# Optimization experiments

Hardware: AMD Instinct MI355X
Metric: run time of the kernel (lower is better)

The kernel has to match this reference:

```python
import math
import jax, jax.numpy as jnp
import numpy as np

B, V, D, H, DE, DFF = 2, 2048, 1024, 16, 256, 4096
DK = D // H


def setup_inputs() -> dict:
    key = jax.random.key(0)
    ks = jax.random.split(key, 24)
    n = lambda k, shape, s=0.02: (jax.random.normal(k, shape, jnp.float32) * s)
    z = lambda *shape: jnp.zeros(shape, jnp.float32)
    return {
        'x': jax.random.normal(ks[0], (B, V, D), jnp.float32),
        'e_node': jax.random.normal(ks[1], (B, V, DE), jnp.float32),
        'conn': jax.random.uniform(ks[2], (B, V, V), jnp.float32),
        'ln1_g': jnp.ones((D,), jnp.float32), 'ln1_b': z(D),
        'f1w1': n(ks[3], (DE, 2 * D)), 'f1b1': z(2 * D),
        'f1w2': n(ks[4], (2 * D, 2 * D)), 'f1b2': z(2 * D),
        'wq': n(ks[5], (D, D)), 'bq': z(D),
        'wk': n(ks[6], (D, D)), 'bk': z(D),
        'wv': n(ks[7], (D, D)), 'bv': z(D),
        'wp': n(ks[8], (D, D)), 'bp': z(D),
        'ln2_g': jnp.ones((D,), jnp.float32), 'ln2_b': z(D),
        'f2w1': n(ks[9], (DE, 2 * D)), 'f2b1': z(2 * D),
        'f2w2': n(ks[10], (2 * D, 2 * D)), 'f2b2': z(2 * D),
        'ffw1': n(ks[11], (D, DFF)), 'ffb1': z(DFF),
        'ffw2': n(ks[12], (DFF, D)), 'ffb2': z(D),
    }


def _ln(x, g, b):
    m = x.mean(-1, keepdims=True)
    v = ((x - m) ** 2).mean(-1, keepdims=True)
    return (x - m) / jnp.sqrt(v + 1e-5) * g + b


def _film(e, w1, b1, w2, b2):
    h = jax.nn.gelu(e @ w1 + b1, approximate=False)  # torch F.gelu default = exact erf
    gb = h @ w2 + b2
    return jnp.split(gb, 2, axis=-1)  # gamma, beta


def reference(x, e_node, conn, ln1_g, ln1_b, f1w1, f1b1, f1w2, f1b2,
              wq, bq, wk, bk, wv, bv, wp, bp, ln2_g, ln2_b,
              f2w1, f2b1, f2w2, f2b2, ffw1, ffb1, ffw2, ffb2):
    b, v, d = x.shape
    # Pre-norm + FiLM 1
    y = _ln(x, ln1_g, ln1_b)
    g1, be1 = _film(e_node, f1w1, f1b1, f1w2, f1b2)
    y = y * (1.0 + g1) + be1
    # Multi-head attention with additive log(conn) mask
    heads = lambda t: t.reshape(b, v, H, DK).transpose(0, 2, 1, 3)  # [B,h,V,dk]
    Q = heads(y @ wq + bq)
    K = heads(y @ wk + bk)
    Vv = heads(y @ wv + bv)
    logits = jnp.einsum('bhqd,bhkd->bhqk', Q, K) / math.sqrt(DK)
    log_mask = jnp.log(jnp.clip(conn, 0.0, 1.0) + 1e-6)[:, None]  # [B,1,V,V]
    s = logits + log_mask
    s = s - s.max(-1, keepdims=True)
    a = jnp.exp(s)
    a = a / (a.sum(-1, keepdims=True) + 1e-8)
    o = jnp.einsum('bhqk,bhkd->bhqd', a, Vv)
    o = o.transpose(0, 2, 1, 3).reshape(b, v, d)
    x = x + (o @ wp + bp)
    # Pre-norm + FiLM 2 + FFN
    y2 = _ln(x, ln2_g, ln2_b)
    g2, be2 = _film(e_node, f2w1, f2b1, f2w2, f2b2)
    y2 = y2 * (1.0 + g2) + be2
    y2 = jax.nn.gelu(y2 @ ffw1 + ffb1, approximate=False) @ ffw2 + ffb2
    return x + y2
```

## Files before the change

### kernel.cpp

```cpp
#include <hip/hip_runtime.h>
#include <math.h>
#include <stdint.h>

#define B_   2
#define V_   2048
#define D_   1024
#define H_   16
#define DK_  64
#define DE_  256
#define DFF_ 4096
#define M_   (B_*V_)
#define D2_  (2*D_)
#define D3_  (3*D_)

typedef unsigned short u16;
typedef unsigned int   u32;
typedef __bf16 bf16x8 __attribute__((ext_vector_type(8)));
typedef u16    u16x8  __attribute__((ext_vector_type(8)));
typedef u16    u16x4  __attribute__((ext_vector_type(4)));
typedef float  f32x4  __attribute__((ext_vector_type(4)));
typedef u32    u32x2  __attribute__((ext_vector_type(2)));
typedef u32    u32x4  __attribute__((ext_vector_type(4)));

__device__ __forceinline__ float bf2f(u16 u) {
    union { unsigned int i; float f; } z; z.i = ((unsigned int)u) << 16; return z.f;
}
__device__ __forceinline__ u16 f2bf(float f) {
    union { float f; unsigned int i; } z; z.f = f;
    unsigned int x = z.i;
    return (u16)((x + 0x7fffu + ((x >> 16) & 1u)) >> 16);
}
__device__ __forceinline__ float gelu_erf(float v) {
    return 0.5f * v * (1.0f + erff(v * 0.70710678118654752f));
}
__device__ __forceinline__ float ldv(const float* p) { return *p; }
__device__ __forceinline__ float ldv(const u16* p)   { return bf2f(*p); }
__device__ __forceinline__ void  stv(float* p, float v) { *p = v; }
__device__ __forceinline__ void  stv(u16* p,   float v) { *p = f2bf(v); }

__device__ __forceinline__ void gload16(const u16* g, u16* lds)
{
    __builtin_amdgcn_global_load_lds(
        (const __attribute__((address_space(1))) void*)g,
        (__attribute__((address_space(3))) void*)(uintptr_t)lds,
        16, 0, 0);
}

__global__ void convT_k(const float* __restrict__ W, u16* __restrict__ Wt, int K, int N)
{
    __shared__ float tile[32][33];
    const int n0 = blockIdx.x * 32, k0 = blockIdx.y * 32;
    const int tx = threadIdx.x, ty = threadIdx.y;
    #pragma unroll
    for (int j = 0; j < 4; ++j)
        tile[ty * 4 + j][tx] = W[(size_t)(k0 + ty * 4 + j) * N + n0 + tx];
    __syncthreads();
    #pragma unroll
    for (int j = 0; j < 4; ++j)
        Wt[(size_t)(n0 + ty * 4 + j) * K + k0 + tx] = f2bf(tile[tx][ty * 4 + j]);
}

__global__ void conv_k(const float* __restrict__ X, u16* __restrict__ Y)
{
    const int i = (blockIdx.x * 256 + threadIdx.x) * 4;
    f32x4 v = *reinterpret_cast<const f32x4*>(X + i);
    u16x4 o;
    #pragma unroll
    for (int j = 0; j < 4; ++j) o[j] = f2bf(v[j]);
    *reinterpret_cast<u16x4*>(Y + i) = o;
}

__global__ void lmask_k(const float* __restrict__ conn, u16* __restrict__ Lm)
{
    const size_t i = ((size_t)blockIdx.x * 256 + threadIdx.x) * 8;
    f32x4 a = *reinterpret_cast<const f32x4*>(conn + i);
    f32x4 b = *reinterpret_cast<const f32x4*>(conn + i + 4);
    u16x8 o;
    #pragma unroll
    for (int j = 0; j < 4; ++j) {
        o[j]     = f2bf(__log2f(fminf(fmaxf(a[j], 0.f), 1.f) + 1e-6f));
        o[j + 4] = f2bf(__log2f(fminf(fmaxf(b[j], 0.f), 1.f) + 1e-6f));
    }
    *reinterpret_cast<u16x8*>(Lm + i) = o;
}

__global__ void qkvbias_k(const float* __restrict__ bq, const float* __restrict__ bk,
                          const float* __restrict__ bv, float* __restrict__ o)
{
    int i = blockIdx.x * 256 + threadIdx.x;
    o[i] = i < 1024 ? bq[i] : (i < 2048 ? bk[i - 1024] : bv[i - 2048]);
}

template<int EPI, typename TC, typename TRES>
__launch_bounds__(256)
__global__ void gemm_k(const u16* __restrict__ A, const u16* __restrict__ Wt,
                       const float* __restrict__ bias, const TRES* __restrict__ res,
                       TC* __restrict__ C, int M, int N, int K)
{
    __shared__ u16 As[128 * 64];
    __shared__ u16 Bs[128 * 64];

    const int tid  = threadIdx.x;
    const int lane = tid & 63;
    const int w    = tid >> 6;
    const int wm   = (w >> 1) * 64, wn = (w & 1) * 64;
    const int m0   = blockIdx.y * 128, n0 = blockIdx.x * 128;
    const int l15  = lane & 15, l4 = lane >> 4;

    int rr[4], cc[4];
    #pragma unroll
    for (int i = 0; i < 4; ++i) {
        rr[i] = w * 32 + i * 8 + (lane >> 3);
        cc[i] = (lane & 7) ^ (rr[i] & 7);
    }

    f32x4 acc[4][4] = {};

    for (int k0 = 0; k0 < K; k0 += 64) {
        if (k0) __syncthreads();
        #pragma unroll
        for (int i = 0; i < 4; ++i) {
            gload16(A  + (size_t)(m0 + rr[i]) * K + k0 + cc[i] * 8, &As[w * 2048 + i * 512]);
            gload16(Wt + (size_t)(n0 + rr[i]) * K + k0 + cc[i] * 8, &Bs[w * 2048 + i * 512]);
        }
        __syncthreads();

        #pragma unroll
        for (int kk = 0; kk < 2; ++kk) {
            bf16x8 a[4], b[4];
            #pragma unroll
            for (int mb = 0; mb < 4; ++mb) {
                int r  = wm + mb * 16 + l15;
                int ph = (kk * 4 + l4) ^ (r & 7);
                a[mb] = *reinterpret_cast<const bf16x8*>(&As[r * 64 + ph * 8]);
            }
            #pragma unroll
            for (int nb = 0; nb < 4; ++nb) {
                int r  = wn + nb * 16 + l15;
                int ph = (kk * 4 + l4) ^ (r & 7);
                b[nb] = *reinterpret_cast<const bf16x8*>(&Bs[r * 64 + ph * 8]);
            }
            #pragma unroll
            for (int mb = 0; mb < 4; ++mb)
                #pragma unroll
                for (int nb = 0; nb < 4; ++nb)
                    acc[mb][nb] = __builtin_amdgcn_mfma_f32_16x16x32_bf16(a[mb], b[nb], acc[mb][nb], 0, 0, 0);
        }
    }

    #pragma unroll
    for (int nb = 0; nb < 4; ++nb) {
        int col = n0 + wn + nb * 16 + l15;
        float bv = bias[col];
        #pragma unroll
        for (int mb = 0; mb < 4; ++mb) {
            #pragma unroll
            for (int i = 0; i < 4; ++i) {
                int row = m0 + wm + mb * 16 + l4 * 4 + i;
                float v = acc[mb][nb][i] + bv;
                if (EPI == 1) v = gelu_erf(v);
                if (EPI == 2) v += ldv(res + (size_t)row * N + col);
                stv(C + (size_t)row * N + col, v);
            }
        }
    }
}

template<typename TX>
__launch_bounds__(256)
__global__ void lnfilm_k(const TX* __restrict__ X, const u16* __restrict__ GB,
                         const float* __restrict__ g, const float* __restrict__ bb,
                         u16* __restrict__ Y)
{
    const int row = blockIdx.x;
    const int tid = threadIdx.x;
    const TX* xr = X + (size_t)row * D_;
    float xs[4], s = 0.f, sq = 0.f;
    #pragma unroll
    for (int j = 0; j < 4; ++j) {
        float v = ldv(xr + tid + j * 256);
        xs[j] = v; s += v; sq += v * v;
    }
    #pragma unroll
    for (int off = 32; off; off >>= 1) {
        s  += __shfl_xor(s, off);
        sq += __shfl_xor(sq, off);
    }
    __shared__ float rs[4], rq[4];
    const int w = tid >> 6;
    if ((tid & 63) == 0) { rs[w] = s; rq[w] = sq; }
    __syncthreads();
    s  = rs[0] + rs[1] + rs[2] + rs[3];
    sq = rq[0] + rq[1] + rq[2] + rq[3];
    const float mean = s * (1.0f / D_);
    const float var  = sq * (1.0f / D_) - mean * mean;
    const float rstd = rsqrtf(fmaxf(var, 0.f) + 1e-5f);
    const u16* gbr = GB + (size_t)row * D2_;
    #pragma unroll
    for (int j = 0; j < 4; ++j) {
        int d = tid + j * 256;
        float v = (xs[j] - mean) * rstd * g[d] + bb[d];
        v = v * (1.0f + bf2f(gbr[d])) + bf2f(gbr[D_ + d]);
        Y[(size_t)row * D_ + d] = f2bf(v);
    }
}

__launch_bounds__(256)
__global__ void attn_k(const u16* __restrict__ Q, const u16* __restrict__ K,
                       const u16* __restrict__ Vv, const u16* __restrict__ Lm,
                       u16* __restrict__ O, int ld)
{
    __shared__ u16 Ks[64 * 64];
    __shared__ u16 Vs[64 * 64];
    __shared__ u16 Lms[64 * 64];
    __shared__ u16 Ps[4 * 16 * 72];

    const int blk = blockIdx.x;
    const int qt  = blk & 31;
    const int h   = (blk >> 5) & 15;
    const int b   = blk >> 9;
    const int q0  = qt * 64;
    const int tid = threadIdx.x, lane = tid & 63, w = tid >> 6;
    const int l15 = lane & 15, l4 = lane >> 4;
    const size_t bV = (size_t)b * V_;

    const u16* qp = Q + (bV + q0 + w * 16 + l15) * ld + h * 64;
    bf16x8 qa[2];
    {
        u16x8 r0 = *reinterpret_cast<const u16x8*>(qp + l4 * 8);
        u16x8 r1 = *reinterpret_cast<const u16x8*>(qp + 32 + l4 * 8);
        u16x8 s0, s1;
        #pragma unroll
        for (int j = 0; j < 8; ++j) {
            s0[j] = f2bf(bf2f(r0[j]) * 0.125f);
            s1[j] = f2bf(bf2f(r1[j]) * 0.125f);
        }
        union { u16x8 u; bf16x8 h; } c0, c1;
        c0.u = s0; c1.u = s1;
        qa[0] = c0.h; qa[1] = c1.h;
    }

    const int rStage = (lane >> 3);
    const int cSw    = ((lane & 7) ^ rStage) * 8;
    const int vK     = ((lane >> 5) << 2) + ((lane & 7) >> 1);
    const int vDk    = ((lane >> 3) & 3) * 16 + (lane & 1) * 8;
    const u32 vaddr  = (u32)(uintptr_t)&Vs[0] + (l4 << 10) + (l15 << 3);

    const int lmRow  = w * 16 + l15;
    const u16* lmBase = &Lms[lmRow * 64 + (l4 & 1) * 4];
    int lmOff[4];
    #pragma unroll
    for (int kb = 0; kb < 4; ++kb)
        lmOff[kb] = ((((kb << 1) | (l4 >> 1)) ^ (lmRow & 7)) << 3);

    u16* psW = &Ps[(w * 16 + l15) * 72 + l4 * 4];
    const float LOG2E = 1.44269504088896f;

    float lrp = 0.f;
    f32x4 o4[4] = {};

    for (int kt = 0; kt < V_ / 64; ++kt) {
        const int k0 = kt * 64;
        if (kt) __syncthreads();
        #pragma unroll
        for (int i = 0; i < 2; ++i) {
            int r  = i * 32 + w * 8 + rStage;
            int kv = i * 32 + w * 8 + vK;
            gload16(K  + (bV + k0 + r)  * ld + h * 64 + cSw,   &Ks[i * 2048 + w * 512]);
            gload16(Vv + (bV + k0 + kv) * ld + h * 64 + vDk,   &Vs[i * 2048 + w * 512]);
            gload16(Lm + (bV + q0 + r) * (size_t)V_ + k0 + cSw, &Lms[i * 2048 + w * 512]);
        }
        __syncthreads();

        f32x4 s[4];
        #pragma unroll
        for (int kb = 0; kb < 4; ++kb) {
            int row = (kb * 16 + l15) * 64;
            bf16x8 k0f = *reinterpret_cast<const bf16x8*>(&Ks[row + ((l4 ^ (l15 & 7)) * 8)]);
            bf16x8 k1f = *reinterpret_cast<const bf16x8*>(&Ks[row + (((l4 + 4) ^ (l15 & 7)) * 8)]);
            f32x4 z = {};
            z = __builtin_amdgcn_mfma_f32_16x16x32_bf16(k0f, qa[0], z, 0, 0, 0);
            z = __builtin_amdgcn_mfma_f32_16x16x32_bf16(k1f, qa[1], z, 0, 0, 0);
            s[kb] = z;
        }
        #pragma unroll
        for (int kb = 0; kb < 4; ++kb) {
            u16x4 lm4 = *reinterpret_cast<const u16x4*>(lmBase + lmOff[kb]);
            float p0, p1, p2, p3;
            float t0 = fmaf(s[kb][0], LOG2E, bf2f(lm4[0]));
            float t1 = fmaf(s[kb][1], LOG2E, bf2f(lm4[1]));
            float t2 = fmaf(s[kb][2], LOG2E, bf2f(lm4[2]));
            float t3 = fmaf(s[kb][3], LOG2E, bf2f(lm4[3]));
            asm("v_exp_f32 %0, %1" : "=v"(p0) : "v"(t0));
            asm("v_exp_f32 %0, %1" : "=v"(p1) : "v"(t1));
            asm("v_exp_f32 %0, %1" : "=v"(p2) : "v"(t2));
            asm("v_exp_f32 %0, %1" : "=v"(p3) : "v"(t3));
            lrp += (p0 + p1) + (p2 + p3);
            u32 d0, d1;
            asm("v_cvt_pk_bf16_f32 %0, %1, %2" : "=v"(d0) : "v"(p0), "v"(p1));
            asm("v_cvt_pk_bf16_f32 %0, %1, %2" : "=v"(d1) : "v"(p2), "v"(p3));
            u32x2 dd = {d0, d1};
            *reinterpret_cast<u32x2*>(psW + kb * 16) = dd;
        }
        #pragma unroll
        for (int c2 = 0; c2 < 2; ++c2) {
            bf16x8 pa = *reinterpret_cast<const bf16x8*>(&Ps[(w * 16 + l15) * 72 + c2 * 32 + l4 * 8]);
            u32 a0 = vaddr + c2 * 4096;
            u32x2 t0, t1, t2, t3, t4, t5, t6, t7;
            asm volatile("ds_read_b64_tr_b16 %0, %1"            : "=v"(t0) : "v"(a0));
            asm volatile("ds_read_b64_tr_b16 %0, %1 offset:512" : "=v"(t1) : "v"(a0));
            asm volatile("ds_read_b64_tr_b16 %0, %1 offset:128" : "=v"(t2) : "v"(a0));
            asm volatile("ds_read_b64_tr_b16 %0, %1 offset:640" : "=v"(t3) : "v"(a0));
            asm volatile("ds_read_b64_tr_b16 %0, %1 offset:256" : "=v"(t4) : "v"(a0));
            asm volatile("ds_read_b64_tr_b16 %0, %1 offset:768" : "=v"(t5) : "v"(a0));
            asm volatile("ds_read_b64_tr_b16 %0, %1 offset:384" : "=v"(t6) : "v"(a0));
            asm volatile("ds_read_b64_tr_b16 %0, %1 offset:896" : "=v"(t7) : "v"(a0));
            asm volatile("s_waitcnt lgkmcnt(0)" ::: "memory");
            __builtin_amdgcn_sched_barrier(0);
            union { u32x4 u; bf16x8 h; } vb0, vb1, vb2, vb3;
            vb0.u = (u32x4){t0.x, t0.y, t1.x, t1.y};
            vb1.u = (u32x4){t2.x, t2.y, t3.x, t3.y};
            vb2.u = (u32x4){t4.x, t4.y, t5.x, t5.y};
            vb3.u = (u32x4){t6.x, t6.y, t7.x, t7.y};
            o4[0] = __builtin_amdgcn_mfma_f32_16x16x32_bf16(pa, vb0.h, o4[0], 0, 0, 0);
            o4[1] = __builtin_amdgcn_mfma_f32_16x16x32_bf16(pa, vb1.h, o4[1], 0, 0, 0);
            o4[2] = __builtin_amdgcn_mfma_f32_16x16x32_bf16(pa, vb2.h, o4[2], 0, 0, 0);
            o4[3] = __builtin_amdgcn_mfma_f32_16x16x32_bf16(pa, vb3.h, o4[3], 0, 0, 0);
        }
    }

    float v = lrp;
    v += __shfl_xor(v, 16);
    v += __shfl_xor(v, 32);
    #pragma unroll
    for (int i = 0; i < 4; ++i) {
        float lw = __shfl(v, (lane & 48) | (((lane >> 4) << 2) + i));
        float rcp = 1.0f / (lw + 1e-8f);
        int q = q0 + w * 16 + l4 * 4 + i;
        u16* op = O + (bV + q) * D_ + h * 64;
        #pragma unroll
        for (int nb = 0; nb < 4; ++nb)
            op[nb * 16 + l15] = f2bf(o4[nb][i] * rcp);
    }
}

extern "C" void kernel_launch(void* const* d_in, const int* in_sizes, int n_in,
                              void* d_out, int out_size, void* d_ws, size_t ws_size,
                              hipStream_t stream)
{
    (void)in_sizes; (void)n_in; (void)out_size; (void)ws_size;
    const float* x    = (const float*)d_in[0];
    const float* e    = (const float*)d_in[1];
    const float* conn = (const float*)d_in[2];
    const float* ln1g = (const float*)d_in[3];
    const float* ln1b = (const float*)d_in[4];
    const float* f1w1 = (const float*)d_in[5];
    const float* f1b1 = (const float*)d_in[6];
    const float* f1w2 = (const float*)d_in[7];
    const float* f1b2 = (const float*)d_in[8];
    const float* wq   = (const float*)d_in[9];
    const float* bq   = (const float*)d_in[10];
    const float* wk   = (const float*)d_in[11];
    const float* bk   = (const float*)d_in[12];
    const float* wv   = (const float*)d_in[13];
    const float* bv   = (const float*)d_in[14];
    const float* wp   = (const float*)d_in[15];
    const float* bp   = (const float*)d_in[16];
    const float* ln2g = (const float*)d_in[17];
    const float* ln2b = (const float*)d_in[18];
    const float* f2w1 = (const float*)d_in[19];
    const float* f2b1 = (const float*)d_in[20];
    const float* f2w2 = (const float*)d_in[21];
    const float* f2b2 = (const float*)d_in[22];
    const float* ffw1 = (const float*)d_in[23];
    const float* ffb1 = (const float*)d_in[24];
    const float* ffw2 = (const float*)d_in[25];
    const float* ffb2 = (const float*)d_in[26];
    float* out = (float*)d_out;

    char* ws = (char*)d_ws;
    const size_t MB = 1u << 20;
    u16*   Lm    = (u16*)(ws + 0);
    u16*   e_bf  = (u16*)(ws + 16 * MB);
    u16*   h     = (u16*)(ws + 18 * MB);
    u16*   wt2   = (u16*)(ws + 34 * MB);
    u16*   wt8   = (u16*)(ws + 36 * MB);
    u16*   gb    = (u16*)(ws + 44 * MB);
    u16*   y     = (u16*)(ws + 60 * MB);
    u16*   wqkvt = (u16*)(ws + 18 * MB);
    u16*   qkv   = (u16*)(ws + 24 * MB);
    float* qkvb  = (float*)(ws + 71 * MB);
    u16*   o     = (u16*)(ws + 48 * MB);
    u16*   xnew  = (u16*)(ws + 64 * MB);
    u16*   h2    = (u16*)(ws + 18 * MB);
    u16*   gb2   = (u16*)(ws + 44 * MB);
    u16*   y2    = (u16*)(ws + 0);
    u16*   ffw1t = (u16*)(ws + 8 * MB);
    u16*   t     = (u16*)(ws + 16 * MB);
    u16*   ffw2t = (u16*)(ws + 48 * MB);

    dim3 blk(256), tblk(32, 8);
    #define CONVT(W, WT, K, N) convT_k<<<dim3((N)/32, (K)/32), tblk, 0, stream>>>(W, WT, K, N)

    conv_k <<<(M_*DE_)/1024, blk, 0, stream>>>(e, e_bf);
    lmask_k<<<(B_*(size_t)V_*V_)/2048, blk, 0, stream>>>(conn, Lm);

    CONVT(f1w1, wt2, DE_, D2_);
    gemm_k<1, u16, u16><<<dim3(D2_/128, M_/128), blk, 0, stream>>>(e_bf, wt2, f1b1, (const u16*)nullptr, h, M_, D2_, DE_);
    CONVT(f1w2, wt8, D2_, D2_);
    gemm_k<0, u16, u16><<<dim3(D2_/128, M_/128), blk, 0, stream>>>(h, wt8, f1b2, (const u16*)nullptr, gb, M_, D2_, D2_);
    lnfilm_k<float><<<M_, blk, 0, stream>>>(x, gb, ln1g, ln1b, y);
    CONVT(wq, wqkvt,                 D_, D_);
    CONVT(wk, wqkvt + 1024 * 1024,   D_, D_);
    CONVT(wv, wqkvt + 2048 * 1024,   D_, D_);
    qkvbias_k<<<D3_/256, blk, 0, stream>>>(bq, bk, bv, qkvb);
    gemm_k<0, u16, u16><<<dim3(D3_/128, M_/128), blk, 0, stream>>>(y, wqkvt, qkvb, (const u16*)nullptr, qkv, M_, D3_, D_);
    attn_k<<<B_*H_*(V_/64), blk, 0, stream>>>(qkv, qkv + 1024, qkv + 2048, Lm, o, D3_);
    CONVT(wp, wt2, D_, D_);
    gemm_k<2, u16, float><<<dim3(D_/128, M_/128), blk, 0, stream>>>(o, wt2, bp, x, xnew, M_, D_, D_);
    CONVT(f2w1, wt2, DE_, D2_);
    gemm_k<1, u16, u16><<<dim3(D2_/128, M_/128), blk, 0, stream>>>(e_bf, wt2, f2b1, (const u16*)nullptr, h2, M_, D2_, DE_);
    CONVT(f2w2, wt8, D2_, D2_);
    gemm_k<0, u16, u16><<<dim3(D2_/128, M_/128), blk, 0, stream>>>(h2, wt8, f2b2, (const u16*)nullptr, gb2, M_, D2_, D2_);
    lnfilm_k<u16><<<M_, blk, 0, stream>>>(xnew, gb2, ln2g, ln2b, y2);
    CONVT(ffw1, ffw1t, D_, DFF_);
    gemm_k<1, u16, u16><<<dim3(DFF_/128, M_/128), blk, 0, stream>>>(y2, ffw1t, ffb1, (const u16*)nullptr, t, M_, DFF_, D_);
    CONVT(ffw2, ffw2t, DFF_, D_);
    gemm_k<2, float, u16><<<dim3(D_/128, M_/128), blk, 0, stream>>>(t, ffw2t, ffb2, xnew, out, M_, D_, DFF_);
    #undef CONVT
}
```

Measured before the change: 421.0 us.

## Double attention query tile to 128 rows and vectorize LN-FiLM loads

Each attention block now processes 128 query rows, with two 16-row groups per wave, instead of 64. Each K/V tile loaded into shared memory is reused across twice as many queries, and the V transposed reads are hoisted out and shared by both groups. This halves K/V global and LDS traffic per query, at the cost of more registers, more shared memory (a larger Lm and P buffer) and half as many blocks (512), which lowers occupancy. The LN+FiLM kernel also switches to contiguous 4-element vector loads and stores.

```diff
diff --git a/kernel.cpp b/kernel.cpp
--- a/kernel.cpp
+++ b/kernel.cpp
@@ -174,12 +174,17 @@
 {
     const int row = blockIdx.x;
     const int tid = threadIdx.x;
-    const TX* xr = X + (size_t)row * D_;
+    const int d0  = tid * 4;
+    const TX* xr = X + (size_t)row * D_ + d0;
     float xs[4], s = 0.f, sq = 0.f;
-    #pragma unroll
-    for (int j = 0; j < 4; ++j) {
-        float v = ldv(xr + tid + j * 256);
-        xs[j] = v; s += v; sq += v * v;
+    if constexpr (sizeof(TX) == 4) {
+        f32x4 v4 = *reinterpret_cast<const f32x4*>(xr);
+        #pragma unroll
+        for (int j = 0; j < 4; ++j) { xs[j] = v4[j]; s += xs[j]; sq += xs[j] * xs[j]; }
+    } else {
+        u16x4 v4 = *reinterpret_cast<const u16x4*>(xr);
+        #pragma unroll
+        for (int j = 0; j < 4; ++j) { xs[j] = bf2f(v4[j]); s += xs[j]; sq += xs[j] * xs[j]; }
     }
     #pragma unroll
     for (int off = 32; off; off >>= 1) {
@@ -195,14 +200,19 @@
     const float mean = s * (1.0f / D_);
     const float var  = sq * (1.0f / D_) - mean * mean;
     const float rstd = rsqrtf(fmaxf(var, 0.f) + 1e-5f);
-    const u16* gbr = GB + (size_t)row * D2_;
+    const u16* gbr = GB + (size_t)row * D2_ + d0;
+    u16x4 g4 = *reinterpret_cast<const u16x4*>(gbr);
+    u16x4 b4 = *reinterpret_cast<const u16x4*>(gbr + D_);
+    f32x4 gg = *reinterpret_cast<const f32x4*>(g + d0);
+    f32x4 bv = *reinterpret_cast<const f32x4*>(bb + d0);
+    u16x4 o;
     #pragma unroll
     for (int j = 0; j < 4; ++j) {
-        int d = tid + j * 256;
-        float v = (xs[j] - mean) * rstd * g[d] + bb[d];
-        v = v * (1.0f + bf2f(gbr[d])) + bf2f(gbr[D_ + d]);
-        Y[(size_t)row * D_ + d] = f2bf(v);
-    }
+        float v = (xs[j] - mean) * rstd * gg[j] + bv[j];
+        v = v * (1.0f + bf2f(g4[j])) + bf2f(b4[j]);
+        o[j] = f2bf(v);
+    }
+    *reinterpret_cast<u16x4*>(Y + (size_t)row * D_ + d0) = o;
 }
 
 __launch_bounds__(256)
@@ -212,21 +222,22 @@
 {
     __shared__ u16 Ks[64 * 64];
     __shared__ u16 Vs[64 * 64];
-    __shared__ u16 Lms[64 * 64];
-    __shared__ u16 Ps[4 * 16 * 72];
+    __shared__ u16 Lms[128 * 64];
+    __shared__ u16 Ps[128 * 72];
 
     const int blk = blockIdx.x;
-    const int qt  = blk & 31;
-    const int h   = (blk >> 5) & 15;
-    const int b   = blk >> 9;
-    const int q0  = qt * 64;
+    const int qt  = blk & 15;
+    const int h   = (blk >> 4) & 15;
+    const int b   = blk >> 8;
+    const int q0  = qt * 128;
     const int tid = threadIdx.x, lane = tid & 63, w = tid >> 6;
     const int l15 = lane & 15, l4 = lane >> 4;
     const size_t bV = (size_t)b * V_;
 
-    const u16* qp = Q + (bV + q0 + w * 16 + l15) * ld + h * 64;
-    bf16x8 qa[2];
-    {
+    bf16x8 qa[2][2];
+    #pragma unroll
+    for (int g = 0; g < 2; ++g) {
+        const u16* qp = Q + (bV + q0 + w * 32 + g * 16 + l15) * ld + h * 64;
         u16x8 r0 = *reinterpret_cast<const u16x8*>(qp + l4 * 8);
         u16x8 r1 = *reinterpret_cast<const u16x8*>(qp + 32 + l4 * 8);
         u16x8 s0, s1;
@@ -237,7 +248,7 @@
         }
         union { u16x8 u; bf16x8 h; } c0, c1;
         c0.u = s0; c1.u = s1;
-        qa[0] = c0.h; qa[1] = c1.h;
+        qa[g][0] = c0.h; qa[g][1] = c1.h;
     }
 
     const int rStage = (lane >> 3);
@@ -246,18 +257,14 @@
     const int vDk    = ((lane >> 3) & 3) * 16 + (lane & 1) * 8;
     const u32 vaddr  = (u32)(uintptr_t)&Vs[0] + (l4 << 10) + (l15 << 3);
 
-    const int lmRow  = w * 16 + l15;
-    const u16* lmBase = &Lms[lmRow * 64 + (l4 & 1) * 4];
     int lmOff[4];
     #pragma unroll
     for (int kb = 0; kb < 4; ++kb)
-        lmOff[kb] = ((((kb << 1) | (l4 >> 1)) ^ (lmRow & 7)) << 3);
-
-    u16* psW = &Ps[(w * 16 + l15) * 72 + l4 * 4];
+        lmOff[kb] = ((((kb << 1) | (l4 >> 1)) ^ (l15 & 7)) << 3);
+
     const float LOG2E = 1.44269504088896f;
-
-    float lrp = 0.f;
-    f32x4 o4[4] = {};
+    float lrp[2] = {0.f, 0.f};
+    f32x4 o4[2][4] = {};
 
     for (int kt = 0; kt < V_ / 64; ++kt) {
         const int k0 = kt * 64;
@@ -266,45 +273,57 @@
         for (int i = 0; i < 2; ++i) {
             int r  = i * 32 + w * 8 + rStage;
             int kv = i * 32 + w * 8 + vK;
-            gload16(K  + (bV + k0 + r)  * ld + h * 64 + cSw,   &Ks[i * 2048 + w * 512]);
-            gload16(Vv + (bV + k0 + kv) * ld + h * 64 + vDk,   &Vs[i * 2048 + w * 512]);
+            gload16(K  + (bV + k0 + r)  * ld + h * 64 + cSw, &Ks[i * 2048 + w * 512]);
+            gload16(Vv + (bV + k0 + kv) * ld + h * 64 + vDk, &Vs[i * 2048 + w * 512]);
+        }
+        #pragma unroll
+        for (int i = 0; i < 4; ++i) {
+            int r = i * 32 + w * 8 + rStage;
             gload16(Lm + (bV + q0 + r) * (size_t)V_ + k0 + cSw, &Lms[i * 2048 + w * 512]);
         }
         __syncthreads();
 
-        f32x4 s[4];
-        #pragma unroll
-        for (int kb = 0; kb < 4; ++kb) {
-            int row = (kb * 16 + l15) * 64;
-            bf16x8 k0f = *reinterpret_cast<const bf16x8*>(&Ks[row + ((l4 ^ (l15 & 7)) * 8)]);
-            bf16x8 k1f = *reinterpret_cast<const bf16x8*>(&Ks[row + (((l4 + 4) ^ (l15 & 7)) * 8)]);
-            f32x4 z = {};
-            z = __builtin_amdgcn_mfma_f32_16x16x32_bf16(k0f, qa[0], z, 0, 0, 0);
-            z = __builtin_amdgcn_mfma_f32_16x16x32_bf16(k1f, qa[1], z, 0, 0, 0);
-            s[kb] = z;
-        }
-        #pragma unroll
-        for (int kb = 0; kb < 4; ++kb) {
-            u16x4 lm4 = *reinterpret_cast<const u16x4*>(lmBase + lmOff[kb]);
-            float p0, p1, p2, p3;
-            float t0 = fmaf(s[kb][0], LOG2E, bf2f(lm4[0]));
-            float t1 = fmaf(s[kb][1], LOG2E, bf2f(lm4[1]));
-            float t2 = fmaf(s[kb][2], LOG2E, bf2f(lm4[2]));
-            float t3 = fmaf(s[kb][3], LOG2E, bf2f(lm4[3]));
-            asm("v_exp_f32 %0, %1" : "=v"(p0) : "v"(t0));
-            asm("v_exp_f32 %0, %1" : "=v"(p1) : "v"(t1));
-            asm("v_exp_f32 %0, %1" : "=v"(p2) : "v"(t2));
-            asm("v_exp_f32 %0, %1" : "=v"(p3) : "v"(t3));
-            lrp += (p0 + p1) + (p2 + p3);
-            u32 d0, d1;
-            asm("v_cvt_pk_bf16_f32 %0, %1, %2" : "=v"(d0) : "v"(p0), "v"(p1));
-            asm("v_cvt_pk_bf16_f32 %0, %1, %2" : "=v"(d1) : "v"(p2), "v"(p3));
-            u32x2 dd = {d0, d1};
-            *reinterpret_cast<u32x2*>(psW + kb * 16) = dd;
-        }
+        #pragma unroll
+        for (int g = 0; g < 2; ++g) {
+            f32x4 s[4];
+            #pragma unroll
+            for (int kb = 0; kb < 4; ++kb) {
+                int row = (kb * 16 + l15) * 64;
+                bf16x8 k0f = *reinterpret_cast<const bf16x8*>(&Ks[row + ((l4 ^ (l15 & 7)) * 8)]);
+                bf16x8 k1f = *reinterpret_cast<const bf16x8*>(&Ks[row + (((l4 + 4) ^ (l15 & 7)) * 8)]);
+                f32x4 z = {};
+                z = __builtin_amdgcn_mfma_f32_16x16x32_bf16(k0f, qa[g][0], z, 0, 0, 0);
+                z = __builtin_amdgcn_mfma_f32_16x16x32_bf16(k1f, qa[g][1], z, 0, 0, 0);
+                s[kb] = z;
+            }
+            const int lmRow = w * 32 + g * 16 + l15;
+            const u16* lmBase = &Lms[lmRow * 64 + (l4 & 1) * 4];
+            u16* psW = &Ps[lmRow * 72 + l4 * 4];
+            #pragma unroll
+            for (int kb = 0; kb < 4; ++kb) {
+                u16x4 lm4 = *reinterpret_cast<const u16x4*>(lmBase + lmOff[kb]);
+                float p0, p1, p2, p3;
+                float t0 = fmaf(s[kb][0], LOG2E, bf2f(lm4[0]));
+                float t1 = fmaf(s[kb][1], LOG2E, bf2f(lm4[1]));
+                float t2 = fmaf(s[kb][2], LOG2E, bf2f(lm4[2]));
+                float t3 = fmaf(s[kb][3], LOG2E, bf2f(lm4[3]));
+                asm("v_exp_f32 %0, %1" : "=v"(p0) : "v"(t0));
+                asm("v_exp_f32 %0, %1" : "=v"(p1) : "v"(t1));
+                asm("v_exp_f32 %0, %1" : "=v"(p2) : "v"(t2));
+                asm("v_exp_f32 %0, %1" : "=v"(p3) : "v"(t3));
+                lrp[g] += (p0 + p1) + (p2 + p3);
+                u32 d0, d1;
+                asm("v_cvt_pk_bf16_f32 %0, %1, %2" : "=v"(d0) : "v"(p0), "v"(p1));
+                asm("v_cvt_pk_bf16_f32 %0, %1, %2" : "=v"(d1) : "v"(p2), "v"(p3));
+                u32x2 dd = {d0, d1};
+                *reinterpret_cast<u32x2*>(psW + kb * 16) = dd;
+            }
+        }
+
+        union VU { u32x4 u; bf16x8 h; };
+        VU vb[2][4];
         #pragma unroll
         for (int c2 = 0; c2 < 2; ++c2) {
-            bf16x8 pa = *reinterpret_cast<const bf16x8*>(&Ps[(w * 16 + l15) * 72 + c2 * 32 + l4 * 8]);
             u32 a0 = vaddr + c2 * 4096;
             u32x2 t0, t1, t2, t3, t4, t5, t6, t7;
             asm volatile("ds_read_b64_tr_b16 %0, %1"            : "=v"(t0) : "v"(a0));
@@ -317,30 +336,39 @@
             asm volatile("ds_read_b64_tr_b16 %0, %1 offset:896" : "=v"(t7) : "v"(a0));
             asm volatile("s_waitcnt lgkmcnt(0)" ::: "memory");
             __builtin_amdgcn_sched_barrier(0);
-            union { u32x4 u; bf16x8 h; } vb0, vb1, vb2, vb3;
-            vb0.u = (u32x4){t0.x, t0.y, t1.x, t1.y};
-            vb1.u = (u32x4){t2.x, t2.y, t3.x, t3.y};
-            vb2.u = (u32x4){t4.x, t4.y, t5.x, t5.y};
-            vb3.u = (u32x4){t6.x, t6.y, t7.x, t7.y};
-            o4[0] = __builtin_amdgcn_mfma_f32_16x16x32_bf16(pa, vb0.h, o4[0], 0, 0, 0);
-            o4[1] = __builtin_amdgcn_mfma_f32_16x16x32_bf16(pa, vb1.h, o4[1], 0, 0, 0);
-            o4[2] = __builtin_amdgcn_mfma_f32_16x16x32_bf16(pa, vb2.h, o4[2], 0, 0, 0);
-            o4[3] = __builtin_amdgcn_mfma_f32_16x16x32_bf16(pa, vb3.h, o4[3], 0, 0, 0);
-        }
-    }
-
-    float v = lrp;
-    v += __shfl_xor(v, 16);
-    v += __shfl_xor(v, 32);
-    #pragma unroll
-    for (int i = 0; i < 4; ++i) {
-        float lw = __shfl(v, (lane & 48) | (((lane >> 4) << 2) + i));
-        float rcp = 1.0f / (lw + 1e-8f);
-        int q = q0 + w * 16 + l4 * 4 + i;
-        u16* op = O + (bV + q) * D_ + h * 64;
-        #pragma unroll
-        for (int nb = 0; nb < 4; ++nb)
-            op[nb * 16 + l15] = f2bf(o4[nb][i] * rcp);
+            vb[c2][0].u = (u32x4){t0.x, t0.y, t1.x, t1.y};
+            vb[c2][1].u = (u32x4){t2.x, t2.y, t3.x, t3.y};
+            vb[c2][2].u = (u32x4){t4.x, t4.y, t5.x, t5.y};
+            vb[c2][3].u = (u32x4){t6.x, t6.y, t7.x, t7.y};
+        }
+        #pragma unroll
+        for (int g = 0; g < 2; ++g) {
+            const u16* pr = &Ps[(w * 32 + g * 16 + l15) * 72];
+            bf16x8 pa0 = *reinterpret_cast<const bf16x8*>(pr + l4 * 8);
+            bf16x8 pa1 = *reinterpret_cast<const bf16x8*>(pr + 32 + l4 * 8);
+            #pragma unroll
+            for (int nb = 0; nb < 4; ++nb) {
+                o4[g][nb] = __builtin_amdgcn_mfma_f32_16x16x32_bf16(pa0, vb[0][nb].h, o4[g][nb], 0, 0, 0);
+                o4[g][nb] = __builtin_amdgcn_mfma_f32_16x16x32_bf16(pa1, vb[1][nb].h, o4[g][nb], 0, 0, 0);
+            }
+        }
+    }
+
+    #pragma unroll
+    for (int g = 0; g < 2; ++g) {
+        float v = lrp[g];
+        v += __shfl_xor(v, 16);
+        v += __shfl_xor(v, 32);
+        #pragma unroll
+        for (int i = 0; i < 4; ++i) {
+            float lw = __shfl(v, (lane & 48) | ((l4 << 2) + i));
+            float rcp = 1.0f / (lw + 1e-8f);
+            int q = q0 + w * 32 + g * 16 + l4 * 4 + i;
+            u16* op = O + (bV + q) * D_ + h * 64;
+            #pragma unroll
+            for (int nb = 0; nb < 4; ++nb)
+                op[nb * 16 + l15] = f2bf(o4[g][nb][i] * rcp);
+        }
     }
 }
 
@@ -415,7 +443,7 @@
     CONVT(wv, wqkvt + 2048 * 1024,   D_, D_);
     qkvbias_k<<<D3_/256, blk, 0, stream>>>(bq, bk, bv, qkvb);
     gemm_k<0, u16, u16><<<dim3(D3_/128, M_/128), blk, 0, stream>>>(y, wqkvt, qkvb, (const u16*)nullptr, qkv, M_, D3_, D_);
-    attn_k<<<B_*H_*(V_/64), blk, 0, stream>>>(qkv, qkv + 1024, qkv + 2048, Lm, o, D3_);
+    attn_k<<<B_*H_*(V_/128), blk, 0, stream>>>(qkv, qkv + 1024, qkv + 2048, Lm, o, D3_);
     CONVT(wp, wt2, D_, D_);
     gemm_k<2, u16, float><<<dim3(D_/128, M_/128), blk, 0, stream>>>(o, wt2, bp, x, xnew, M_, D_, D_);
     CONVT(f2w1, wt2, DE_, D2_);
```

Result: no change. 418.4 us (-0.6%).
